# Performance work log

Measured on AMD Instinct MI355X. Metric: run time of the kernel, lower is better.

The kernel has to match this reference:

```python
import jax, jax.numpy as jnp
import numpy as np

B, S, DIM = 2, 2048, 4096
H, KV = 32, 8
HD = DIM // H          # 128
REP = H // KV          # 4


def _rope_tables(seq_len, head_dim, base=10000.0):
    inv_freq = 1.0 / (base ** (jnp.arange(0, head_dim, 2, dtype=jnp.float32) / head_dim))
    t = jnp.arange(seq_len, dtype=jnp.float32)
    freqs = jnp.outer(t, inv_freq)                      # [S, D/2]
    emb = jnp.concatenate([freqs, freqs], axis=-1)      # [S, D]
    return jnp.cos(emb)[:, None, :], jnp.sin(emb)[:, None, :]  # [S,1,D]


def setup_inputs() -> dict:
    key = jax.random.key(0)
    kx, kq, kk, kv, ko = jax.random.split(key, 5)
    x = jax.random.normal(kx, (B, S, DIM), dtype=jnp.float32)
    cos, sin = _rope_tables(S, HD)
    s = 0.02
    Wq = jax.random.normal(kq, (DIM, H * HD), dtype=jnp.float32) * s
    Wk = jax.random.normal(kk, (DIM, KV * HD), dtype=jnp.float32) * s
    Wv = jax.random.normal(kv, (DIM, KV * HD), dtype=jnp.float32) * s
    Wo = jax.random.normal(ko, (H * HD, DIM), dtype=jnp.float32) * s
    return {"x": x, "cos": cos, "sin": sin, "Wq": Wq, "Wk": Wk, "Wv": Wv, "Wo": Wo}


def _rotate_half(t):
    t1, t2 = jnp.split(t, 2, axis=-1)
    return jnp.concatenate([-t2, t1], axis=-1)


def reference(x, cos, sin, Wq, Wk, Wv, Wo):
    b, s, _ = x.shape
    q = (x @ Wq).reshape(b, s, H, HD)
    k = (x @ Wk).reshape(b, s, KV, HD)
    v = (x @ Wv).reshape(b, s, KV, HD)
    # RoPE (cos/sin broadcast [S,1,D] -> [B,S,H,D])
    q = q * cos + _rotate_half(q) * sin
    k = k * cos + _rotate_half(k) * sin
    # grouped-head attention: avoid materializing repeated K/V
    q = q.reshape(b, s, KV, REP, HD)
    scale = 1.0 / jnp.sqrt(jnp.asarray(HD, dtype=x.dtype))
    scores = jnp.einsum('bqgrd,bkgd->bgrqk', q, k) * scale  # [B,KV,REP,S,S]
    causal = jnp.tril(jnp.ones((s, s), dtype=bool))
    scores = jnp.where(causal, scores, jnp.finfo(scores.dtype).min)
    attn = jax.nn.softmax(scores, axis=-1)
    out = jnp.einsum('bgrqk,bkgd->bqgrd', attn, v)          # [B,S,KV,REP,HD]
    out = out.reshape(b, s, H * HD)
    return out @ Wo
```

## Files before the change

### kernel.cpp

```cpp
#include <hip/hip_runtime.h>
#include <hip/hip_bf16.h>

#define B_   2
#define S_   2048
#define DIM_ 4096
#define H_   32
#define KV_  8
#define HD_  128
#define MROWS_ (B_ * S_)
#define KVD_ (KV_ * HD_)
#define QKVN_ (DIM_ + 2 * KVD_)

typedef __attribute__((ext_vector_type(8))) short short8;
typedef __attribute__((ext_vector_type(4))) float floatx4;

__device__ __forceinline__ unsigned int f2bf(float f) {
    union { float f; unsigned int u; } v; v.f = f;
    unsigned int lsb = (v.u >> 16) & 1u;
    v.u += 0x7fffu + lsb;
    return v.u >> 16;
}
__device__ __forceinline__ unsigned int pack2bf(float lo, float hi) {
    return f2bf(lo) | (f2bf(hi) << 16);
}

__device__ __forceinline__ uint4 load8cvt(const float* __restrict__ src) {
    const float4 a = ((const float4*)src)[0];
    const float4 b = ((const float4*)src)[1];
    uint4 r;
    r.x = pack2bf(a.x, a.y);
    r.y = pack2bf(a.z, a.w);
    r.z = pack2bf(b.x, b.y);
    r.w = pack2bf(b.z, b.w);
    return r;
}

__device__ __forceinline__ void storeC(float* p, float v) { *p = v; }
__device__ __forceinline__ void storeC(__hip_bfloat16* p, float v) { *p = __float2bfloat16(v); }

__device__ __forceinline__ void gload16(const unsigned short* g, unsigned short* l)
{
    __builtin_amdgcn_global_load_lds(
        (const __attribute__((address_space(1))) void*)g,
        (__attribute__((address_space(3))) void*)l,
        16, 0, 0);
}

__global__ __launch_bounds__(256)
void convert_bf16(const float* __restrict__ X, unsigned short* __restrict__ Y, int total8)
{
    const int i = blockIdx.x * 256 + threadIdx.x;
    if (i >= total8) return;
    uint4 v = load8cvt(X + (size_t)i * 8);
    *(uint4*)(Y + (size_t)i * 8) = v;
}

__global__ __launch_bounds__(256)
void wtrans(const float* __restrict__ W, unsigned short* __restrict__ Wt, int K, int N)
{
    __shared__ float tile[64][65];
    const int n0 = blockIdx.x * 64;
    const int k0 = blockIdx.y * 64;
    const int t  = threadIdx.x;
    #pragma unroll
    for (int it = 0; it < 4; ++it) {
        const int seg = t + it * 256;
        const int r   = seg >> 4;
        const int c   = (seg & 15) << 2;
        const float4 v = *(const float4*)&W[(size_t)(k0 + r) * N + n0 + c];
        tile[r][c]     = v.x;
        tile[r][c + 1] = v.y;
        tile[r][c + 2] = v.z;
        tile[r][c + 3] = v.w;
    }
    __syncthreads();
    const int n  = t >> 2;
    const int ks = (t & 3) << 4;
    unsigned int ob[8];
    #pragma unroll
    for (int j = 0; j < 8; ++j)
        ob[j] = pack2bf(tile[ks + 2 * j][n], tile[ks + 2 * j + 1][n]);
    uint4* dst = (uint4*)&Wt[(size_t)(n0 + n) * K + k0 + ks];
    dst[0] = ((const uint4*)ob)[0];
    dst[1] = ((const uint4*)ob)[1];
}

template <typename TC>
__global__ __launch_bounds__(256)
void gemm_bt(const unsigned short* __restrict__ A,
             const unsigned short* __restrict__ Bt,
             TC* __restrict__ C,
             int M, int N, int K)
{
    __shared__ unsigned short As[128 * 32];
    __shared__ unsigned short Bs[128 * 32];

    const int tid  = threadIdx.x;
    const int lane = tid & 63;
    const int w    = tid >> 6;
    const int wm   = (w >> 1) * 64;
    const int wn   = (w & 1) * 64;

    const int gx  = gridDim.x;
    const int nwg = gx * gridDim.y;
    int lid = blockIdx.y * gx + blockIdx.x;
    if ((nwg & 7) == 0) {
        const int q = nwg >> 3;
        lid = (lid & 7) * q + (lid >> 3);
    }
    const int m0 = (lid / gx) * 128;
    const int n0 = (lid % gx) * 128;

    const int fm   = lane & 15;
    const int fk   = (lane >> 4) * 8;

    floatx4 acc[4][4] = {};

    const int sr = tid >> 2;
    const int sk = (tid & 3) * 8;
    const unsigned short* ga0 = A  + (size_t)(m0 + sr) * K + sk;
    const unsigned short* ga1 = ga0 + (size_t)64 * K;
    const unsigned short* gb0 = Bt + (size_t)(n0 + sr) * K + sk;
    const unsigned short* gb1 = gb0 + (size_t)64 * K;
    unsigned short* lA = As + w * 512;
    unsigned short* lB = Bs + w * 512;

    for (int k0 = 0; k0 < K; k0 += 32) {
        gload16(ga0 + k0, lA);
        gload16(ga1 + k0, lA + 2048);
        gload16(gb0 + k0, lB);
        gload16(gb1 + k0, lB + 2048);
        __syncthreads();

        short8 af[4], bf[4];
        #pragma unroll
        for (int i = 0; i < 4; ++i) {
            af[i] = *(const short8*)&As[(wm + i * 16 + fm) * 32 + fk];
            bf[i] = *(const short8*)&Bs[(wn + i * 16 + fm) * 32 + fk];
        }
        #pragma unroll
        for (int mi = 0; mi < 4; ++mi)
            #pragma unroll
            for (int ni = 0; ni < 4; ++ni)
                acc[mi][ni] = __builtin_amdgcn_mfma_f32_16x16x32_bf16(
                    af[mi], bf[ni], acc[mi][ni], 0, 0, 0);
        __syncthreads();
    }

    const int cl = lane & 15;
    const int rq = (lane >> 4) * 4;
    #pragma unroll
    for (int mi = 0; mi < 4; ++mi) {
        #pragma unroll
        for (int ni = 0; ni < 4; ++ni) {
            const int col = n0 + wn + ni * 16 + cl;
            #pragma unroll
            for (int r = 0; r < 4; ++r) {
                const int row = m0 + wm + mi * 16 + rq + r;
                storeC(C + (size_t)row * N + col, acc[mi][ni][r]);
            }
        }
    }
}

__global__ void rope_kernel(unsigned short* __restrict__ T,
                            const float* __restrict__ cosb,
                            const float* __restrict__ sinb,
                            int NH, int coloff, int total)
{
    int idx = blockIdx.x * blockDim.x + threadIdx.x;
    if (idx >= total) return;
    const int dh   = idx & 63;
    const int rest = idx >> 6;
    const int h    = rest % NH;
    const int bs   = rest / NH;
    const int s    = bs & (S_ - 1);
    const size_t base = (size_t)bs * QKVN_ + coloff + h * HD_;
    union { unsigned short u; __hip_bfloat16 b; } c1v, c2v;
    const float t1 = __bfloat162float(*(__hip_bfloat16*)&T[base + dh]);
    const float t2 = __bfloat162float(*(__hip_bfloat16*)&T[base + dh + 64]);
    const float c1 = cosb[s * HD_ + dh];
    const float s1 = sinb[s * HD_ + dh];
    const float c2 = cosb[s * HD_ + dh + 64];
    const float s2 = sinb[s * HD_ + dh + 64];
    T[base + dh]      = (unsigned short)f2bf(t1 * c1 - t2 * s1);
    T[base + dh + 64] = (unsigned short)f2bf(t2 * c2 + t1 * s2);
    (void)c1v; (void)c2v;
}

__global__ __launch_bounds__(256)
void attn_mfma(const unsigned short* __restrict__ QKV,
               __hip_bfloat16* __restrict__ O)
{
    const int qt = (int)gridDim.x - 1 - (int)blockIdx.x;
    const int bh = blockIdx.y;
    const int b  = bh >> 5;
    const int h  = bh & 31;
    const int g  = h >> 2;
    const int q0 = qt * 128;

    __shared__ unsigned short Ks[64][136];
    __shared__ unsigned short Vt[128][72];
    __shared__ unsigned short Ps[4][32][72];

    const int tid  = threadIdx.x;
    const int lane = tid & 63;
    const int w    = tid >> 6;
    const int fm   = lane & 15;
    const int quad = lane >> 4;
    const int fk   = quad * 8;

    const int qrow_base = q0 + w * 32;

    short8 qf[2][4];
    #pragma unroll
    for (int mt = 0; mt < 2; ++mt) {
        const int row = qrow_base + mt * 16 + fm;
        const unsigned short* qp = QKV + (size_t)(b * S_ + row) * QKVN_ + h * HD_;
        #pragma unroll
        for (int dt = 0; dt < 4; ++dt)
            qf[mt][dt] = *(const short8*)(qp + dt * 32 + fk);
    }

    floatx4 o_acc[2][8] = {};
    float m_r[2][4], l_r[2][4];
    #pragma unroll
    for (int mt = 0; mt < 2; ++mt)
        #pragma unroll
        for (int r = 0; r < 4; ++r) { m_r[mt][r] = -1e30f; l_r[mt][r] = 0.f; }

    const float scale = 0.08838834764831845f;

    const int key  = tid >> 2;
    const int d0   = (tid & 3) * 32;
    const int vcol = key ^ ((tid & 3) << 4);
    const unsigned short* Kp = QKV + DIM_ + g * HD_;
    const unsigned short* Vp = QKV + DIM_ + KVD_ + g * HD_;
    const size_t gbase = (size_t)(b * S_ + key) * QKVN_ + d0;
    const size_t gstep = (size_t)64 * QKVN_;
    uint4 kreg[4], vreg[4];

    const int ktiles = 2 * (qt + 1);
    {
        const uint4* kp = (const uint4*)(Kp + gbase);
        const uint4* vp = (const uint4*)(Vp + gbase);
        #pragma unroll
        for (int i = 0; i < 4; ++i) { kreg[i] = kp[i]; vreg[i] = vp[i]; }
    }
    for (int kt = 0; kt < ktiles; ++kt) {
        const int k0 = kt * 64;
        __syncthreads();
        {
            *(uint4*)&Ks[key][d0]      = kreg[0];
            *(uint4*)&Ks[key][d0 + 8]  = kreg[1];
            *(uint4*)&Ks[key][d0 + 16] = kreg[2];
            *(uint4*)&Ks[key][d0 + 24] = kreg[3];
            const unsigned short* vs = (const unsigned short*)vreg;
            #pragma unroll
            for (int i = 0; i < 32; ++i)
                Vt[d0 + i][vcol] = vs[i];
        }
        __syncthreads();
        if (kt + 1 < ktiles) {
            const uint4* kp = (const uint4*)(Kp + gbase + (size_t)(kt + 1) * gstep);
            const uint4* vp = (const uint4*)(Vp + gbase + (size_t)(kt + 1) * gstep);
            #pragma unroll
            for (int i = 0; i < 4; ++i) { kreg[i] = kp[i]; vreg[i] = vp[i]; }
        }

        floatx4 s_acc[2][4] = {};
        #pragma unroll
        for (int dt = 0; dt < 4; ++dt) {
            #pragma unroll
            for (int nt = 0; nt < 4; ++nt) {
                short8 bfr = *(const short8*)&Ks[nt * 16 + fm][dt * 32 + fk];
                #pragma unroll
                for (int mt = 0; mt < 2; ++mt)
                    s_acc[mt][nt] = __builtin_amdgcn_mfma_f32_16x16x32_bf16(
                        qf[mt][dt], bfr, s_acc[mt][nt], 0, 0, 0);
            }
        }

        #pragma unroll
        for (int mt = 0; mt < 2; ++mt) {
            const int rowq0 = qrow_base + mt * 16 + quad * 4;
            #pragma unroll
            for (int r = 0; r < 4; ++r) {
                const int rowq = rowq0 + r;
                float mx = -1e30f;
                #pragma unroll
                for (int nt = 0; nt < 4; ++nt) {
                    const int c = k0 + nt * 16 + fm;
                    float s = s_acc[mt][nt][r] * scale;
                    s = (c <= rowq) ? s : -1e30f;
                    s_acc[mt][nt][r] = s;
                    mx = fmaxf(mx, s);
                }
                #pragma unroll
                for (int off = 1; off < 16; off <<= 1)
                    mx = fmaxf(mx, __shfl_xor(mx, off));
                const float mold = m_r[mt][r];
                const float mnew = fmaxf(mold, mx);
                const float alpha = __expf(mold - mnew);
                float rsum = 0.f;
                #pragma unroll
                for (int nt = 0; nt < 4; ++nt) {
                    const float p = __expf(s_acc[mt][nt][r] - mnew);
                    s_acc[mt][nt][r] = p;
                    rsum += p;
                }
                #pragma unroll
                for (int off = 1; off < 16; off <<= 1)
                    rsum += __shfl_xor(rsum, off);
                m_r[mt][r] = mnew;
                l_r[mt][r] = l_r[mt][r] * alpha + rsum;
                #pragma unroll
                for (int nt = 0; nt < 8; ++nt)
                    o_acc[mt][nt][r] *= alpha;
                #pragma unroll
                for (int nt = 0; nt < 4; ++nt)
                    Ps[w][mt * 16 + quad * 4 + r][(nt * 16 + fm) ^ (quad << 3)] =
                        (unsigned short)f2bf(s_acc[mt][nt][r]);
            }
        }

        #pragma unroll
        for (int ct = 0; ct < 2; ++ct) {
            short8 af[2];
            #pragma unroll
            for (int mt = 0; mt < 2; ++mt)
                af[mt] = *(const short8*)
                    &Ps[w][mt * 16 + fm][ct * 32 + ((quad ^ (fm >> 2)) << 3)];
            #pragma unroll
            for (int nt = 0; nt < 8; ++nt) {
                short8 bfr = *(const short8*)
                    &Vt[nt * 16 + fm][(ct * 32 + fk) ^ ((nt >> 1) << 4)];
                #pragma unroll
                for (int mt = 0; mt < 2; ++mt)
                    o_acc[mt][nt] = __builtin_amdgcn_mfma_f32_16x16x32_bf16(
                        af[mt], bfr, o_acc[mt][nt], 0, 0, 0);
            }
        }
    }

    #pragma unroll
    for (int mt = 0; mt < 2; ++mt) {
        #pragma unroll
        for (int r = 0; r < 4; ++r) {
            const int row = qrow_base + mt * 16 + quad * 4 + r;
            const float inv_l = 1.f / l_r[mt][r];
            __hip_bfloat16* op = O + ((size_t)(b * S_ + row) * H_ + h) * HD_;
            #pragma unroll
            for (int nt = 0; nt < 8; ++nt)
                op[nt * 16 + fm] = __float2bfloat16(o_acc[mt][nt][r] * inv_l);
        }
    }
}

extern "C" void kernel_launch(void* const* d_in, const int* in_sizes, int n_in,
                              void* d_out, int out_size, void* d_ws, size_t ws_size,
                              hipStream_t stream)
{
    const float* x    = (const float*)d_in[0];
    const float* cosb = (const float*)d_in[1];
    const float* sinb = (const float*)d_in[2];
    const float* Wq   = (const float*)d_in[3];
    const float* Wk   = (const float*)d_in[4];
    const float* Wv   = (const float*)d_in[5];
    const float* Wo   = (const float*)d_in[6];
    float* out = (float*)d_out;

    char* ws = (char*)d_ws;
    const size_t MB = 1024 * 1024;
    unsigned short* Xb  = (unsigned short*)(ws);
    unsigned short* Ab  = (unsigned short*)(ws);
    unsigned short* WT  = (unsigned short*)(ws + 32 * MB);
    unsigned short* WoT = (unsigned short*)(ws + 32 * MB);
    unsigned short* QKV = (unsigned short*)(ws + 80 * MB);

    unsigned short* WTq = WT;
    unsigned short* WTk = WT + (size_t)DIM_ * DIM_;
    unsigned short* WTv = WT + (size_t)(DIM_ + KVD_) * DIM_;

    dim3 blk(256);

    convert_bf16<<<dim3((MROWS_ * DIM_) / 8 / 256), blk, 0, stream>>>(
        x, Xb, (MROWS_ * DIM_) / 8);

    wtrans<<<dim3(DIM_ / 64, DIM_ / 64), blk, 0, stream>>>(Wq, WTq, DIM_, DIM_);
    wtrans<<<dim3(KVD_ / 64, DIM_ / 64), blk, 0, stream>>>(Wk, WTk, DIM_, KVD_);
    wtrans<<<dim3(KVD_ / 64, DIM_ / 64), blk, 0, stream>>>(Wv, WTv, DIM_, KVD_);

    gemm_bt<__hip_bfloat16><<<dim3(QKVN_ / 128, MROWS_ / 128), blk, 0, stream>>>(
        Xb, WT, (__hip_bfloat16*)QKV, MROWS_, QKVN_, DIM_);

    wtrans<<<dim3(DIM_ / 64, DIM_ / 64), blk, 0, stream>>>(Wo, WoT, DIM_, DIM_);

    {
        int totq = MROWS_ * H_ * 64;
        int totk = MROWS_ * KV_ * 64;
        rope_kernel<<<(totq + 255) / 256, blk, 0, stream>>>(
            QKV, cosb, sinb, H_, 0, totq);
        rope_kernel<<<(totk + 255) / 256, blk, 0, stream>>>(
            QKV, cosb, sinb, KV_, DIM_, totk);
    }

    attn_mfma<<<dim3(S_ / 128, B_ * H_), blk, 0, stream>>>(
        QKV, (__hip_bfloat16*)Ab);

    gemm_bt<float><<<dim3(DIM_ / 128, MROWS_ / 128), blk, 0, stream>>>(
        Ab, WoT, out, MROWS_, DIM_, DIM_);
}
```

Before: 1.104 ms.

## Pair causal query tiles per block and streamline attention softmax and output stores

```diff
diff --git a/kernel.cpp b/kernel.cpp
--- a/kernel.cpp
+++ b/kernel.cpp
@@ -176,7 +176,6 @@
     const int bs   = rest / NH;
     const int s    = bs & (S_ - 1);
     const size_t base = (size_t)bs * QKVN_ + coloff + h * HD_;
-    union { unsigned short u; __hip_bfloat16 b; } c1v, c2v;
     const float t1 = __bfloat162float(*(__hip_bfloat16*)&T[base + dh]);
     const float t2 = __bfloat162float(*(__hip_bfloat16*)&T[base + dh + 64]);
     const float c1 = cosb[s * HD_ + dh];
@@ -185,23 +184,23 @@
     const float s2 = sinb[s * HD_ + dh + 64];
     T[base + dh]      = (unsigned short)f2bf(t1 * c1 - t2 * s1);
     T[base + dh + 64] = (unsigned short)f2bf(t2 * c2 + t1 * s2);
-    (void)c1v; (void)c2v;
 }
 
 __global__ __launch_bounds__(256)
 void attn_mfma(const unsigned short* __restrict__ QKV,
                __hip_bfloat16* __restrict__ O)
 {
-    const int qt = (int)gridDim.x - 1 - (int)blockIdx.x;
+    const int bx = blockIdx.x;
     const int bh = blockIdx.y;
     const int b  = bh >> 5;
     const int h  = bh & 31;
     const int g  = h >> 2;
-    const int q0 = qt * 128;
-
-    __shared__ unsigned short Ks[64][136];
-    __shared__ unsigned short Vt[128][72];
-    __shared__ unsigned short Ps[4][32][72];
+
+    __shared__ unsigned short lds[27136];
+    unsigned short* KsF = lds;
+    unsigned short* VtF = lds + 8704;
+    unsigned short* PsF = lds + 17920;
+    unsigned short* Es  = lds;
 
     const int tid  = threadIdx.x;
     const int lane = tid & 63;
@@ -210,26 +209,10 @@
     const int quad = lane >> 4;
     const int fk   = quad * 8;
 
-    const int qrow_base = q0 + w * 32;
-
-    short8 qf[2][4];
+    const float scale = 0.08838834764831845f;
+    short8 ones;
     #pragma unroll
-    for (int mt = 0; mt < 2; ++mt) {
-        const int row = qrow_base + mt * 16 + fm;
-        const unsigned short* qp = QKV + (size_t)(b * S_ + row) * QKVN_ + h * HD_;
-        #pragma unroll
-        for (int dt = 0; dt < 4; ++dt)
-            qf[mt][dt] = *(const short8*)(qp + dt * 32 + fk);
-    }
-
-    floatx4 o_acc[2][8] = {};
-    float m_r[2][4], l_r[2][4];
-    #pragma unroll
-    for (int mt = 0; mt < 2; ++mt)
-        #pragma unroll
-        for (int r = 0; r < 4; ++r) { m_r[mt][r] = -1e30f; l_r[mt][r] = 0.f; }
-
-    const float scale = 0.08838834764831845f;
+    for (int j = 0; j < 8; ++j) ones[j] = (short)0x3F80;
 
     const int key  = tid >> 2;
     const int d0   = (tid & 3) * 32;
@@ -240,119 +223,165 @@
     const size_t gstep = (size_t)64 * QKVN_;
     uint4 kreg[4], vreg[4];
 
-    const int ktiles = 2 * (qt + 1);
-    {
-        const uint4* kp = (const uint4*)(Kp + gbase);
-        const uint4* vp = (const uint4*)(Vp + gbase);
-        #pragma unroll
-        for (int i = 0; i < 4; ++i) { kreg[i] = kp[i]; vreg[i] = vp[i]; }
-    }
-    for (int kt = 0; kt < ktiles; ++kt) {
-        const int k0 = kt * 64;
+    for (int pass = 0; pass < 2; ++pass) {
+        const int qt = pass ? bx : (15 - bx);
+        const int q0 = qt * 128;
+        const int qrow_base = q0 + w * 32;
+
+        short8 qf[2][4];
+        #pragma unroll
+        for (int mt = 0; mt < 2; ++mt) {
+            const int row = qrow_base + mt * 16 + fm;
+            const unsigned short* qp = QKV + (size_t)(b * S_ + row) * QKVN_ + h * HD_;
+            #pragma unroll
+            for (int dt = 0; dt < 4; ++dt)
+                qf[mt][dt] = *(const short8*)(qp + dt * 32 + fk);
+        }
+
+        floatx4 o_acc[2][8] = {};
+        floatx4 sum_acc[2] = {};
+        float m_r[2][4];
+        #pragma unroll
+        for (int mt = 0; mt < 2; ++mt)
+            #pragma unroll
+            for (int r = 0; r < 4; ++r) m_r[mt][r] = -1e30f;
+
+        const int ktiles = 2 * (qt + 1);
+        {
+            const uint4* kp = (const uint4*)(Kp + gbase);
+            const uint4* vp = (const uint4*)(Vp + gbase);
+            #pragma unroll
+            for (int i = 0; i < 4; ++i) { kreg[i] = kp[i]; vreg[i] = vp[i]; }
+        }
+
+        for (int kt = 0; kt < ktiles; ++kt) {
+            const int k0 = kt * 64;
+            __syncthreads();
+            {
+                *(uint4*)&KsF[key * 136 + d0]      = kreg[0];
+                *(uint4*)&KsF[key * 136 + d0 + 8]  = kreg[1];
+                *(uint4*)&KsF[key * 136 + d0 + 16] = kreg[2];
+                *(uint4*)&KsF[key * 136 + d0 + 24] = kreg[3];
+                const unsigned short* vs = (const unsigned short*)vreg;
+                #pragma unroll
+                for (int i = 0; i < 32; ++i)
+                    VtF[(d0 + i) * 72 + vcol] = vs[i];
+            }
+            __syncthreads();
+            if (kt + 1 < ktiles) {
+                const uint4* kp = (const uint4*)(Kp + gbase + (size_t)(kt + 1) * gstep);
+                const uint4* vp = (const uint4*)(Vp + gbase + (size_t)(kt + 1) * gstep);
+                #pragma unroll
+                for (int i = 0; i < 4; ++i) { kreg[i] = kp[i]; vreg[i] = vp[i]; }
+            }
+
+            if (k0 > qrow_base + 31) continue;
+
+            floatx4 s_acc[2][4] = {};
+            #pragma unroll
+            for (int dt = 0; dt < 4; ++dt) {
+                #pragma unroll
+                for (int nt = 0; nt < 4; ++nt) {
+                    short8 bfr = *(const short8*)&KsF[(nt * 16 + fm) * 136 + dt * 32 + fk];
+                    #pragma unroll
+                    for (int mt = 0; mt < 2; ++mt)
+                        s_acc[mt][nt] = __builtin_amdgcn_mfma_f32_16x16x32_bf16(
+                            qf[mt][dt], bfr, s_acc[mt][nt], 0, 0, 0);
+                }
+            }
+
+            const bool needmask = (k0 + 63 > qrow_base);
+            #pragma unroll
+            for (int mt = 0; mt < 2; ++mt) {
+                const int rowq0 = qrow_base + mt * 16 + quad * 4;
+                #pragma unroll
+                for (int r = 0; r < 4; ++r) {
+                    if (needmask) {
+                        const int rowq = rowq0 + r;
+                        #pragma unroll
+                        for (int nt = 0; nt < 4; ++nt) {
+                            const int c = k0 + nt * 16 + fm;
+                            if (c > rowq) s_acc[mt][nt][r] = -1e30f;
+                        }
+                    }
+                    float mx = fmaxf(fmaxf(s_acc[mt][0][r], s_acc[mt][1][r]),
+                                     fmaxf(s_acc[mt][2][r], s_acc[mt][3][r]));
+                    #pragma unroll
+                    for (int off = 1; off < 16; off <<= 1)
+                        mx = fmaxf(mx, __shfl_xor(mx, off));
+                    float mcur = m_r[mt][r];
+                    if (__any(mx > mcur + 90.5f)) {
+                        const float mnew = fmaxf(mcur, mx);
+                        const float alpha = __expf((mcur - mnew) * scale);
+                        #pragma unroll
+                        for (int nt = 0; nt < 8; ++nt)
+                            o_acc[mt][nt][r] *= alpha;
+                        sum_acc[mt][r] *= alpha;
+                        m_r[mt][r] = mnew;
+                        mcur = mnew;
+                    }
+                    const int prow = mt * 16 + quad * 4 + r;
+                    #pragma unroll
+                    for (int nt = 0; nt < 4; ++nt) {
+                        const float p = __expf((s_acc[mt][nt][r] - mcur) * scale);
+                        PsF[(w * 32 + prow) * 72 + ((nt * 16 + fm) ^ (quad << 3))] =
+                            (unsigned short)f2bf(p);
+                    }
+                }
+            }
+
+            #pragma unroll
+            for (int ct = 0; ct < 2; ++ct) {
+                short8 af[2];
+                #pragma unroll
+                for (int mt = 0; mt < 2; ++mt)
+                    af[mt] = *(const short8*)
+                        &PsF[(w * 32 + mt * 16 + fm) * 72 + ct * 32 + ((quad ^ (fm >> 2)) << 3)];
+                #pragma unroll
+                for (int mt = 0; mt < 2; ++mt)
+                    sum_acc[mt] = __builtin_amdgcn_mfma_f32_16x16x32_bf16(
+                        af[mt], ones, sum_acc[mt], 0, 0, 0);
+                #pragma unroll
+                for (int nt = 0; nt < 8; ++nt) {
+                    short8 bfr = *(const short8*)
+                        &VtF[(nt * 16 + fm) * 72 + ((ct * 32 + fk) ^ ((nt >> 1) << 4))];
+                    #pragma unroll
+                    for (int mt = 0; mt < 2; ++mt)
+                        o_acc[mt][nt] = __builtin_amdgcn_mfma_f32_16x16x32_bf16(
+                            af[mt], bfr, o_acc[mt][nt], 0, 0, 0);
+                }
+            }
+        }
+
         __syncthreads();
-        {
-            *(uint4*)&Ks[key][d0]      = kreg[0];
-            *(uint4*)&Ks[key][d0 + 8]  = kreg[1];
-            *(uint4*)&Ks[key][d0 + 16] = kreg[2];
-            *(uint4*)&Ks[key][d0 + 24] = kreg[3];
-            const unsigned short* vs = (const unsigned short*)vreg;
-            #pragma unroll
-            for (int i = 0; i < 32; ++i)
-                Vt[d0 + i][vcol] = vs[i];
+        unsigned short* Ew = Es + w * (32 * 136);
+        #pragma unroll
+        for (int mt = 0; mt < 2; ++mt) {
+            #pragma unroll
+            for (int r = 0; r < 4; ++r) {
+                const float inv_l = 1.f / sum_acc[mt][r];
+                const int prow = mt * 16 + quad * 4 + r;
+                #pragma unroll
+                for (int nt = 0; nt < 8; ++nt)
+                    Ew[prow * 136 + nt * 16 + fm] =
+                        (unsigned short)f2bf(o_acc[mt][nt][r] * inv_l);
+            }
         }
         __syncthreads();
-        if (kt + 1 < ktiles) {
-            const uint4* kp = (const uint4*)(Kp + gbase + (size_t)(kt + 1) * gstep);
-            const uint4* vp = (const uint4*)(Vp + gbase + (size_t)(kt + 1) * gstep);
-            #pragma unroll
-            for (int i = 0; i < 4; ++i) { kreg[i] = kp[i]; vreg[i] = vp[i]; }
-        }
-
-        floatx4 s_acc[2][4] = {};
-        #pragma unroll
-        for (int dt = 0; dt < 4; ++dt) {
-            #pragma unroll
-            for (int nt = 0; nt < 4; ++nt) {
-                short8 bfr = *(const short8*)&Ks[nt * 16 + fm][dt * 32 + fk];
-                #pragma unroll
-                for (int mt = 0; mt < 2; ++mt)
-                    s_acc[mt][nt] = __builtin_amdgcn_mfma_f32_16x16x32_bf16(
-                        qf[mt][dt], bfr, s_acc[mt][nt], 0, 0, 0);
-            }
-        }
-
         #pragma unroll
         for (int mt = 0; mt < 2; ++mt) {
-            const int rowq0 = qrow_base + mt * 16 + quad * 4;
-            #pragma unroll
-            for (int r = 0; r < 4; ++r) {
-                const int rowq = rowq0 + r;
-                float mx = -1e30f;
-                #pragma unroll
-                for (int nt = 0; nt < 4; ++nt) {
-                    const int c = k0 + nt * 16 + fm;
-                    float s = s_acc[mt][nt][r] * scale;
-                    s = (c <= rowq) ? s : -1e30f;
-                    s_acc[mt][nt][r] = s;
-                    mx = fmaxf(mx, s);
-                }
-                #pragma unroll
-                for (int off = 1; off < 16; off <<= 1)
-                    mx = fmaxf(mx, __shfl_xor(mx, off));
-                const float mold = m_r[mt][r];
-                const float mnew = fmaxf(mold, mx);
-                const float alpha = __expf(mold - mnew);
-                float rsum = 0.f;
-                #pragma unroll
-                for (int nt = 0; nt < 4; ++nt) {
-                    const float p = __expf(s_acc[mt][nt][r] - mnew);
-                    s_acc[mt][nt][r] = p;
-                    rsum += p;
-                }
-                #pragma unroll
-                for (int off = 1; off < 16; off <<= 1)
-                    rsum += __shfl_xor(rsum, off);
-                m_r[mt][r] = mnew;
-                l_r[mt][r] = l_r[mt][r] * alpha + rsum;
-                #pragma unroll
-                for (int nt = 0; nt < 8; ++nt)
-                    o_acc[mt][nt][r] *= alpha;
-                #pragma unroll
-                for (int nt = 0; nt < 4; ++nt)
-                    Ps[w][mt * 16 + quad * 4 + r][(nt * 16 + fm) ^ (quad << 3)] =
-                        (unsigned short)f2bf(s_acc[mt][nt][r]);
-            }
-        }
-
-        #pragma unroll
-        for (int ct = 0; ct < 2; ++ct) {
-            short8 af[2];
-            #pragma unroll
-            for (int mt = 0; mt < 2; ++mt)
-                af[mt] = *(const short8*)
-                    &Ps[w][mt * 16 + fm][ct * 32 + ((quad ^ (fm >> 2)) << 3)];
-            #pragma unroll
-            for (int nt = 0; nt < 8; ++nt) {
-                short8 bfr = *(const short8*)
-                    &Vt[nt * 16 + fm][(ct * 32 + fk) ^ ((nt >> 1) << 4)];
-                #pragma unroll
-                for (int mt = 0; mt < 2; ++mt)
-                    o_acc[mt][nt] = __builtin_amdgcn_mfma_f32_16x16x32_bf16(
-                        af[mt], bfr, o_acc[mt][nt], 0, 0, 0);
-            }
-        }
-    }
-
-    #pragma unroll
-    for (int mt = 0; mt < 2; ++mt) {
-        #pragma unroll
-        for (int r = 0; r < 4; ++r) {
-            const int row = qrow_base + mt * 16 + quad * 4 + r;
-            const float inv_l = 1.f / l_r[mt][r];
-            __hip_bfloat16* op = O + ((size_t)(b * S_ + row) * H_ + h) * HD_;
-            #pragma unroll
-            for (int nt = 0; nt < 8; ++nt)
-                op[nt * 16 + fm] = __float2bfloat16(o_acc[mt][nt][r] * inv_l);
+            const int rowE = mt * 16 + fm;
+            const unsigned short* src = Ew + rowE * 136 + quad * 32;
+            __hip_bfloat16* op = O + ((size_t)(b * S_ + qrow_base + rowE) * H_ + h) * HD_
+                                   + quad * 32;
+            uint4 v0 = *(const uint4*)(src);
+            uint4 v1 = *(const uint4*)(src + 8);
+            uint4 v2 = *(const uint4*)(src + 16);
+            uint4 v3 = *(const uint4*)(src + 24);
+            *(uint4*)(op)      = v0;
+            *(uint4*)(op + 8)  = v1;
+            *(uint4*)(op + 16) = v2;
+            *(uint4*)(op + 24) = v3;
         }
     }
 }
@@ -405,7 +434,7 @@
             QKV, cosb, sinb, KV_, DIM_, totk);
     }
 
-    attn_mfma<<<dim3(S_ / 128, B_ * H_), blk, 0, stream>>>(
+    attn_mfma<<<dim3(8, B_ * H_), blk, 0, stream>>>(
         QKV, (__hip_bfloat16*)Ab);
 
     gemm_bt<float><<<dim3(DIM_ / 128, MROWS_ / 128), blk, 0, stream>>>(
```

Result: no change. 1.101 ms (-0.3%).
